# Optimization experiments

Measured on AMD Instinct MI355X. Metric: run time of the kernel, lower is better.

Reference implementation:

```python
import jax, jax.numpy as jnp
import numpy as np

N_NODES = 50000
N_EDGES = 600000
IN_C, HID, OUT_C, HEADS = 128, 64, 16, 4


def setup_inputs() -> dict:
    key = jax.random.key(0)
    ks = jax.random.split(key, 12)
    s = 1.0 / np.sqrt(HID)
    return {
        "x": jax.random.normal(ks[0], (N_NODES, IN_C), dtype=jnp.float32),
        "edge_index": jax.random.randint(ks[1], (2, N_EDGES), 0, N_NODES, dtype=jnp.int64),
        "W_lin": jax.random.normal(ks[2], (IN_C, HID), dtype=jnp.float32) / np.sqrt(IN_C),
        "b_lin": jnp.zeros((HID,), dtype=jnp.float32),
        "Wq": jax.random.normal(ks[3], (HID, HID), dtype=jnp.float32) * s,
        "bq": jnp.zeros((HID,), dtype=jnp.float32),
        "Wk": jax.random.normal(ks[4], (HID, HID), dtype=jnp.float32) * s,
        "bk": jnp.zeros((HID,), dtype=jnp.float32),
        "Wv": jax.random.normal(ks[5], (HID, HID), dtype=jnp.float32) * s,
        "bv": jnp.zeros((HID,), dtype=jnp.float32),
        "W_out": jax.random.normal(ks[6], (HID, OUT_C), dtype=jnp.float32) * s,
        "b_out": jnp.zeros((OUT_C,), dtype=jnp.float32),
    }


def _dna_conv(xs, src, dst, norm, Wq, bq, Wk, bk, Wv, bv):
    # xs: [N, L, C] stacked layer histories. Multi-head attention per edge:
    # query = target node's latest layer, keys/values = source node's full history.
    N, L, C = xs.shape
    d = C // HEADS
    q = (xs[:, -1] @ Wq + bq).reshape(N, HEADS, d)          # [N,H,d]
    k = (xs @ Wk + bk).reshape(N, L, HEADS, d)               # [N,L,H,d]
    v = (xs @ Wv + bv).reshape(N, L, HEADS, d)
    scores = jnp.einsum('ehd,elhd->ehl', q[dst], k[src]) / jnp.sqrt(jnp.float32(d))
    attn = jax.nn.softmax(scores, axis=-1)                   # softmax over layer history
    msg = jnp.einsum('ehl,elhd->ehd', attn, v[src]).reshape(-1, C)  # [E,C]
    msg = msg * norm[:, None]                                # GCN symmetric norm
    return jax.ops.segment_sum(msg, dst, num_segments=N)


def reference(x, edge_index, W_lin, b_lin, Wq, bq, Wk, bk, Wv, bv, W_out, b_out):
    N = x.shape[0]
    loop = jnp.arange(N, dtype=edge_index.dtype)
    src = jnp.concatenate([edge_index[0], loop])
    dst = jnp.concatenate([edge_index[1], loop])
    deg = jax.ops.segment_sum(jnp.ones_like(dst, dtype=x.dtype), dst, num_segments=N)
    dinv = jnp.where(deg > 0, jax.lax.rsqrt(jnp.maximum(deg, 1.0)), 0.0)
    norm = dinv[src] * dinv[dst]

    h = x @ W_lin + b_lin                                    # [N,HID]
    xs = h[:, None, :]
    for _ in range(3):
        out = _dna_conv(xs, src, dst, norm, Wq, bq, Wk, bk, Wv, bv)
        xs = jnp.concatenate([xs, out[:, None, :]], axis=1)
    return xs[:, -1] @ W_out + b_out                          # [N,OUT_C]
```

## Files before the change

### kernel.cpp

```cpp
#include <hip/hip_runtime.h>


__device__ inline unsigned short bf16_rne(float f) {
    unsigned int u = __float_as_uint(f);
    unsigned int r = u + 0x7FFFu + ((u >> 16) & 1u);
    return (unsigned short)(r >> 16);
}

__global__ __launch_bounds__(256) void hist_dst_k(const int* __restrict__ dst,
                                                  int* __restrict__ cnt, int E) {
    int e = blockIdx.x * 256 + threadIdx.x;
    if (e < E) atomicAdd(&cnt[dst[e]], 1);
}

__global__ __launch_bounds__(256) void scan1_k(const int* __restrict__ cnt,
                                               int* __restrict__ excl,
                                               int* __restrict__ aux,
                                               float* __restrict__ dinv, int N) {
    __shared__ int wtot[4];
    int b = blockIdx.x, t = threadIdx.x;
    int lane = t & 63, w = t >> 6;
    int base = b * 1024 + t * 4;
    int v0 = (base + 0 < N) ? cnt[base + 0] + 1 : 0;
    int v1 = (base + 1 < N) ? cnt[base + 1] + 1 : 0;
    int v2 = (base + 2 < N) ? cnt[base + 2] + 1 : 0;
    int v3 = (base + 3 < N) ? cnt[base + 3] + 1 : 0;
    if (base + 0 < N) dinv[base + 0] = rsqrtf((float)v0);
    if (base + 1 < N) dinv[base + 1] = rsqrtf((float)v1);
    if (base + 2 < N) dinv[base + 2] = rsqrtf((float)v2);
    if (base + 3 < N) dinv[base + 3] = rsqrtf((float)v3);
    int s = v0 + v1 + v2 + v3;
    int incl = s;
#pragma unroll
    for (int off = 1; off < 64; off <<= 1) {
        int u = __shfl_up(incl, off);
        if (lane >= off) incl += u;
    }
    if (lane == 63) wtot[w] = incl;
    __syncthreads();
    int wb = 0;
#pragma unroll
    for (int j = 0; j < 4; ++j) if (j < w) wb += wtot[j];
    int ex = wb + incl - s;
    if (base + 0 < N) excl[base + 0] = ex;
    if (base + 1 < N) excl[base + 1] = ex + v0;
    if (base + 2 < N) excl[base + 2] = ex + v0 + v1;
    if (base + 3 < N) excl[base + 3] = ex + v0 + v1 + v2;
    if (t == 0) aux[b] = wtot[0] + wtot[1] + wtot[2] + wtot[3];
}

__global__ __launch_bounds__(64) void scan_aux_k(int* __restrict__ aux, int nb,
                                                 int* __restrict__ total) {
    int lane = threadIdx.x;
    int v = (lane < nb) ? aux[lane] : 0;
    int incl = v;
#pragma unroll
    for (int off = 1; off < 64; off <<= 1) {
        int u = __shfl_up(incl, off);
        if (lane >= off) incl += u;
    }
    if (lane < nb) aux[lane] = incl - v;
    if (lane == 63) total[0] = incl;
}

__global__ __launch_bounds__(256) void scan_add_k(int* __restrict__ offs,
                                                  const int* __restrict__ aux,
                                                  int* __restrict__ cursor, int N) {
    int i = blockIdx.x * 256 + threadIdx.x;
    if (i < N) {
        int o = offs[i] + aux[i >> 10];
        offs[i] = o;
        cursor[i] = o;
    }
}

__global__ __launch_bounds__(256) void scatter_dst_k(const int* __restrict__ src,
                                                     const int* __restrict__ dst,
                                                     int* __restrict__ cursor,
                                                     int* __restrict__ src_sorted,
                                                     int E, int N) {
    int e = blockIdx.x * 256 + threadIdx.x;
    int M = E + N;
    if (e >= M) return;
    int s, d;
    if (e < E) { s = src[e]; d = dst[e]; }
    else       { s = d = e - E; }
    int pos = atomicAdd(&cursor[d], 1);
    src_sorted[pos] = s;
}

__global__ __launch_bounds__(256) void lin128_64_k(const float* __restrict__ x,
                                                   const float* __restrict__ W,
                                                   const float* __restrict__ b,
                                                   float* __restrict__ y, int N) {
    __shared__ float sW[128 * 64];
    __shared__ float sb[64];
    for (int i = threadIdx.x; i < 128 * 64; i += 256) sW[i] = W[i];
    if (threadIdx.x < 64) sb[threadIdx.x] = b[threadIdx.x];
    __syncthreads();
    int w = threadIdx.x >> 6, c = threadIdx.x & 63;
    int r0 = blockIdx.x * 16 + w * 4;
    if (r0 >= N) return;
    const float* xr[4];
#pragma unroll
    for (int j = 0; j < 4; ++j) {
        int r = r0 + j; if (r > N - 1) r = N - 1;
        xr[j] = x + (size_t)r * 128;
    }
    float acc[4];
#pragma unroll
    for (int j = 0; j < 4; ++j) acc[j] = sb[c];
    for (int k = 0; k < 128; ++k) {
        float wv = sW[k * 64 + c];
#pragma unroll
        for (int j = 0; j < 4; ++j) acc[j] = fmaf(xr[j][k], wv, acc[j]);
    }
#pragma unroll
    for (int j = 0; j < 4; ++j) {
        int r = r0 + j;
        if (r < N) y[(size_t)r * 64 + c] = acc[j];
    }
}

__global__ __launch_bounds__(1024) void qkv_pack0_k(const float* __restrict__ h,
                                                    const float* __restrict__ Wq, const float* __restrict__ bq,
                                                    const float* __restrict__ Wk, const float* __restrict__ bk,
                                                    const float* __restrict__ Wv, const float* __restrict__ bv,
                                                    const float* __restrict__ dinv,
                                                    float* __restrict__ q,
                                                    unsigned int* __restrict__ PL,
                                                    unsigned short* __restrict__ V0,
                                                    int N) {
    __shared__ float sW[3 * 64 * 64];
    __shared__ float rowS[16][64];
    int tid = threadIdx.x;
    for (int i = tid; i < 4096; i += 1024) {
        sW[i] = Wq[i]; sW[4096 + i] = Wk[i]; sW[8192 + i] = Wv[i];
    }
    __syncthreads();
    int w = tid >> 6, lane = tid & 63;
    int r = blockIdx.x * 16 + w;
    if (r >= N) return;
    rowS[w][lane] = h[(size_t)r * 64 + lane];
    float dr = dinv[r];
    float aq = bq[lane], ak = bk[lane], av = bv[lane];
#pragma unroll 8
    for (int k = 0; k < 64; ++k) {
        float xk = rowS[w][k];
        aq = fmaf(xk, sW[k * 64 + lane], aq);
        ak = fmaf(xk, sW[4096 + k * 64 + lane], ak);
        av = fmaf(xk, sW[8192 + k * 64 + lane], av);
    }
    q[(size_t)r * 64 + lane] = aq;
    unsigned short vb = bf16_rne(av * dr);
    PL[(size_t)r * 192 + lane] = (unsigned int)bf16_rne(ak) | ((unsigned int)vb << 16);
    V0[(size_t)r * 64 + lane] = vb;
}

template <int L, bool EMIT_OUT>
__global__ __launch_bounds__(1024) void attn_fused_k(const int* __restrict__ offs,
                                                     const int* __restrict__ src_sorted,
                                                     const float* __restrict__ dinv,
                                                     float* __restrict__ q,
                                                     unsigned int* __restrict__ PL,
                                                     const unsigned short* __restrict__ V0,
                                                     const float* __restrict__ WA, const float* __restrict__ bA,
                                                     const float* __restrict__ Wk, const float* __restrict__ bk,
                                                     const float* __restrict__ Wv, const float* __restrict__ bv,
                                                     float* __restrict__ out, int N) {
    constexpr int SWSZ = EMIT_OUT ? (64 * 16) : (3 * 64 * 64);
    __shared__ float sW[SWSZ];
    __shared__ float rowS[16][64];
    int tid = threadIdx.x;
    if (EMIT_OUT) {
        for (int i = tid; i < 64 * 16; i += 1024) sW[i] = WA[i];
    } else {
        for (int i = tid; i < 4096; i += 1024) {
            sW[i] = WA[i]; sW[4096 + i] = Wk[i]; sW[8192 + i] = Wv[i];
        }
    }
    __syncthreads();
    int w = tid >> 6, lane = tid & 63;
    int d = blockIdx.x * 16 + w;
    if (d >= N) return;

    int beg = offs[d], end = offs[d + 1];
    float qv = (L > 1) ? q[(size_t)d * 64 + lane] : 0.0f;
    float acc = 0.0f;

    for (int base = beg; base < end; base += 64) {
        int m = end - base;
        if (m > 64) m = 64;
        int sid = (base + lane < end) ? src_sorted[base + lane] : 0;
#pragma unroll 4
        for (int i = 0; i < m; ++i) {
            int s = __shfl(sid, i);
            if (L == 1) {
                acc += __uint_as_float((unsigned int)V0[(size_t)s * 64 + lane] << 16);
            } else if (L == 2) {
                const unsigned int* p = PL + (size_t)s * 192;
                unsigned int u0 = p[lane];
                unsigned int u1 = p[64 + lane];
                float k0 = __uint_as_float((u0 & 0xFFFFu) << 16);
                float v0 = __uint_as_float(u0 & 0xFFFF0000u);
                float k1 = __uint_as_float((u1 & 0xFFFFu) << 16);
                float v1 = __uint_as_float(u1 & 0xFFFF0000u);
                float p0 = qv * k0;
                float p1 = qv * k1;
#pragma unroll
                for (int mk = 8; mk >= 1; mk >>= 1) {
                    p0 += __shfl_xor(p0, mk);
                    p1 += __shfl_xor(p1, mk);
                }
                float e  = __expf((p1 - p0) * 0.25f);
                float w0 = __builtin_amdgcn_rcpf(1.0f + e);
                float w1 = 1.0f - w0;
                acc = fmaf(w0, v0, acc);
                acc = fmaf(w1, v1, acc);
            } else {
                const unsigned int* p = PL + (size_t)s * 192;
                unsigned int u0 = p[lane];
                unsigned int u1 = p[64 + lane];
                unsigned int u2 = p[128 + lane];
                float k0 = __uint_as_float((u0 & 0xFFFFu) << 16);
                float v0 = __uint_as_float(u0 & 0xFFFF0000u);
                float k1 = __uint_as_float((u1 & 0xFFFFu) << 16);
                float v1 = __uint_as_float(u1 & 0xFFFF0000u);
                float k2 = __uint_as_float((u2 & 0xFFFFu) << 16);
                float v2 = __uint_as_float(u2 & 0xFFFF0000u);
                float p0 = qv * k0;
                float p1 = qv * k1;
                float p2 = qv * k2;
#pragma unroll
                for (int mk = 8; mk >= 1; mk >>= 1) {
                    p0 += __shfl_xor(p0, mk);
                    p1 += __shfl_xor(p1, mk);
                    p2 += __shfl_xor(p2, mk);
                }
                float s0 = p0 * 0.25f, s1 = p1 * 0.25f, s2 = p2 * 0.25f;
                float mx = fmaxf(fmaxf(s0, s1), s2);
                float w0 = __expf(s0 - mx);
                float w1 = __expf(s1 - mx);
                float w2 = __expf(s2 - mx);
                float inv = __builtin_amdgcn_rcpf(w0 + w1 + w2);
                float msg = w0 * v0;
                msg = fmaf(w1, v1, msg);
                msg = fmaf(w2, v2, msg);
                acc = fmaf(msg, inv, acc);
            }
        }
    }

    float dr = dinv[d];
    float rv = acc * dr;
    rowS[w][lane] = rv;

    if (EMIT_OUT) {
        int co = lane & 15;
        float ao = bA[co];
#pragma unroll 8
        for (int k = 0; k < 64; ++k) ao = fmaf(rowS[w][k], sW[k * 16 + co], ao);
        if (lane < 16) out[(size_t)d * 16 + co] = ao;
    } else {
        float aq = bA[lane], ak = bk[lane], av = bv[lane];
#pragma unroll 8
        for (int k = 0; k < 64; ++k) {
            float xk = rowS[w][k];
            aq = fmaf(xk, sW[k * 64 + lane], aq);
            ak = fmaf(xk, sW[4096 + k * 64 + lane], ak);
            av = fmaf(xk, sW[8192 + k * 64 + lane], av);
        }
        q[(size_t)d * 64 + lane] = aq;
        PL[(size_t)d * 192 + L * 64 + lane] =
            (unsigned int)bf16_rne(ak) | ((unsigned int)bf16_rne(av * dr) << 16);
    }
}

extern "C" void kernel_launch(void* const* d_in, const int* in_sizes, int n_in,
                              void* d_out, int out_size, void* d_ws, size_t ws_size,
                              hipStream_t stream) {
    const float* x     = (const float*)d_in[0];
    const int*   ei    = (const int*)d_in[1];
    const float* W_lin = (const float*)d_in[2];
    const float* b_lin = (const float*)d_in[3];
    const float* Wq    = (const float*)d_in[4];
    const float* bq    = (const float*)d_in[5];
    const float* Wk    = (const float*)d_in[6];
    const float* bk    = (const float*)d_in[7];
    const float* Wv    = (const float*)d_in[8];
    const float* bv    = (const float*)d_in[9];
    const float* W_out = (const float*)d_in[10];
    const float* b_out = (const float*)d_in[11];
    float* out = (float*)d_out;

    const int N = in_sizes[0] / 128;
    const int E = in_sizes[1] / 2;
    const int M = E + N;
    const int* srcp = ei;
    const int* dstp = ei + E;

    char* wsb = (char*)d_ws;
    float*          dinv       = (float*)wsb;           wsb += (size_t)N * sizeof(float);
    int*            cnt        = (int*)wsb;             wsb += (size_t)N * sizeof(int);
    int*            offs       = (int*)wsb;             wsb += (size_t)(N + 1) * sizeof(int);
    int*            cursor     = (int*)wsb;             wsb += (size_t)N * sizeof(int);
    int*            aux        = (int*)wsb;             wsb += 64 * sizeof(int);
    int*            src_sorted = (int*)wsb;             wsb += (size_t)M * sizeof(int);
    float*          qb         = (float*)wsb;           wsb += (size_t)N * 64 * sizeof(float);
    unsigned int*   PL         = (unsigned int*)wsb;    wsb += (size_t)N * 192 * sizeof(unsigned int);
    unsigned short* V0p        = (unsigned short*)wsb;  wsb += (size_t)N * 64 * sizeof(unsigned short);
    float*          hA         = (float*)wsb;

    const int gN   = (N + 255) / 256;
    const int gE   = (E + 255) / 256;
    const int gM   = (M + 255) / 256;
    const int g16  = (N + 15) / 16;
    const int nb   = (N + 1023) / 1024;

    hipMemsetAsync(cnt, 0, (size_t)N * sizeof(int), stream);
    hist_dst_k<<<gE, 256, 0, stream>>>(dstp, cnt, E);
    scan1_k<<<nb, 256, 0, stream>>>(cnt, offs, aux, dinv, N);
    scan_aux_k<<<1, 64, 0, stream>>>(aux, nb, offs + N);
    scan_add_k<<<gN, 256, 0, stream>>>(offs, aux, cursor, N);
    scatter_dst_k<<<gM, 256, 0, stream>>>(srcp, dstp, cursor, src_sorted, E, N);

    lin128_64_k<<<g16, 256, 0, stream>>>(x, W_lin, b_lin, hA, N);
    qkv_pack0_k<<<g16, 1024, 0, stream>>>(hA, Wq, bq, Wk, bk, Wv, bv, dinv,
                                          qb, PL, V0p, N);

    attn_fused_k<1, false><<<g16, 1024, 0, stream>>>(offs, src_sorted, dinv, qb, PL, V0p,
                                                     Wq, bq, Wk, bk, Wv, bv, out, N);
    attn_fused_k<2, false><<<g16, 1024, 0, stream>>>(offs, src_sorted, dinv, qb, PL, V0p,
                                                     Wq, bq, Wk, bk, Wv, bv, out, N);
    attn_fused_k<3, true><<<g16, 1024, 0, stream>>>(offs, src_sorted, dinv, qb, PL, V0p,
                                                    W_out, b_out, Wk, bk, Wv, bv, out, N);
}
```

Before: 510.0 us.

## Switch to edge-parallel strip attention with atomics and separate projection kernels

Replaces the per-destination-wavefront fused attention+projection kernels with an edge-strip kernel. Each 16-lane group processes 8 consecutive sorted edges using vectorized uint4 loads and 4-lane head reductions, flushing partial sums with float atomics when the destination changes. The QKV projections move to a separate register-resident-weight kernel using readlane broadcasts, with the query scale folded into q. The output projection also becomes its own kernel. The aim is to balance load across skewed degrees and widen memory accesses. The cost is extra kernels, memsets, a dst_sorted array and atomic traffic.

Measured after the change: 691.7 us. 1.36x slower.

```diff
diff --git a/kernel.cpp b/kernel.cpp
--- a/kernel.cpp
+++ b/kernel.cpp
@@ -1,11 +1,15 @@
 #include <hip/hip_runtime.h>
 
+
+#define SEDGE 8
 
 __device__ inline unsigned short bf16_rne(float f) {
     unsigned int u = __float_as_uint(f);
     unsigned int r = u + 0x7FFFu + ((u >> 16) & 1u);
     return (unsigned short)(r >> 16);
 }
+__device__ inline float kf(unsigned int u) { return __uint_as_float(u << 16); }
+__device__ inline float vf(unsigned int u) { return __uint_as_float(u & 0xFFFF0000u); }
 
 __global__ __launch_bounds__(256) void hist_dst_k(const int* __restrict__ dst,
                                                   int* __restrict__ cnt, int E) {
@@ -78,6 +82,7 @@
                                                      const int* __restrict__ dst,
                                                      int* __restrict__ cursor,
                                                      int* __restrict__ src_sorted,
+                                                     int* __restrict__ dst_sorted,
                                                      int E, int N) {
     int e = blockIdx.x * 256 + threadIdx.x;
     int M = E + N;
@@ -87,6 +92,7 @@
     else       { s = d = e - E; }
     int pos = atomicAdd(&cursor[d], 1);
     src_sorted[pos] = s;
+    dst_sorted[pos] = d;
 }
 
 __global__ __launch_bounds__(256) void lin128_64_k(const float* __restrict__ x,
@@ -122,158 +128,167 @@
     }
 }
 
-__global__ __launch_bounds__(1024) void qkv_pack0_k(const float* __restrict__ h,
-                                                    const float* __restrict__ Wq, const float* __restrict__ bq,
-                                                    const float* __restrict__ Wk, const float* __restrict__ bk,
-                                                    const float* __restrict__ Wv, const float* __restrict__ bv,
+template <bool WRITE_V0>
+__global__ __launch_bounds__(192) void proj_qkv_k(const float* __restrict__ X,
+                                                  const float* __restrict__ Wq, const float* __restrict__ bq,
+                                                  const float* __restrict__ Wk, const float* __restrict__ bk,
+                                                  const float* __restrict__ Wv, const float* __restrict__ bv,
+                                                  const float* __restrict__ dinv,
+                                                  float* __restrict__ q,
+                                                  unsigned int* __restrict__ PL,
+                                                  unsigned short* __restrict__ V0,
+                                                  int N, int l, int RPB) {
+    int w = threadIdx.x >> 6;
+    int c = threadIdx.x & 63;
+    const float* W = (w == 0) ? Wq : (w == 1) ? Wk : Wv;
+    const float* B = (w == 0) ? bq : (w == 1) ? bk : bv;
+    float wr[64];
+#pragma unroll
+    for (int k = 0; k < 64; ++k) wr[k] = W[k * 64 + c];
+    float bias = B[c];
+    int r0 = blockIdx.x * RPB;
+    int r1 = r0 + RPB; if (r1 > N) r1 = N;
+    unsigned short* PLh = (unsigned short*)PL;
+    for (int r = r0; r < r1; ++r) {
+        float xv = X[(size_t)r * 64 + c];
+        float a = bias;
+#pragma unroll
+        for (int k = 0; k < 64; ++k) {
+            float xk = __int_as_float(__builtin_amdgcn_readlane(__float_as_int(xv), k));
+            a = fmaf(xk, wr[k], a);
+        }
+        if (w == 0) {
+            q[(size_t)r * 64 + c] = a * 0.25f;
+        } else if (w == 1) {
+            PLh[((size_t)r * 192 + l * 64 + c) * 2] = bf16_rne(a);
+        } else {
+            unsigned short vb = bf16_rne(a * dinv[r]);
+            PLh[((size_t)r * 192 + l * 64 + c) * 2 + 1] = vb;
+            if (WRITE_V0) V0[(size_t)r * 64 + c] = vb;
+        }
+    }
+}
+
+template <int L>
+__global__ __launch_bounds__(256) void attn_strip_k(const int* __restrict__ src_sorted,
+                                                    const int* __restrict__ dst_sorted,
                                                     const float* __restrict__ dinv,
-                                                    float* __restrict__ q,
-                                                    unsigned int* __restrict__ PL,
-                                                    unsigned short* __restrict__ V0,
-                                                    int N) {
-    __shared__ float sW[3 * 64 * 64];
-    __shared__ float rowS[16][64];
-    int tid = threadIdx.x;
-    for (int i = tid; i < 4096; i += 1024) {
-        sW[i] = Wq[i]; sW[4096 + i] = Wk[i]; sW[8192 + i] = Wv[i];
-    }
-    __syncthreads();
-    int w = tid >> 6, lane = tid & 63;
-    int r = blockIdx.x * 16 + w;
-    if (r >= N) return;
-    rowS[w][lane] = h[(size_t)r * 64 + lane];
-    float dr = dinv[r];
-    float aq = bq[lane], ak = bk[lane], av = bv[lane];
-#pragma unroll 8
-    for (int k = 0; k < 64; ++k) {
-        float xk = rowS[w][k];
-        aq = fmaf(xk, sW[k * 64 + lane], aq);
-        ak = fmaf(xk, sW[4096 + k * 64 + lane], ak);
-        av = fmaf(xk, sW[8192 + k * 64 + lane], av);
-    }
-    q[(size_t)r * 64 + lane] = aq;
-    unsigned short vb = bf16_rne(av * dr);
-    PL[(size_t)r * 192 + lane] = (unsigned int)bf16_rne(ak) | ((unsigned int)vb << 16);
-    V0[(size_t)r * 64 + lane] = vb;
-}
-
-template <int L, bool EMIT_OUT>
-__global__ __launch_bounds__(1024) void attn_fused_k(const int* __restrict__ offs,
-                                                     const int* __restrict__ src_sorted,
-                                                     const float* __restrict__ dinv,
-                                                     float* __restrict__ q,
-                                                     unsigned int* __restrict__ PL,
-                                                     const unsigned short* __restrict__ V0,
-                                                     const float* __restrict__ WA, const float* __restrict__ bA,
-                                                     const float* __restrict__ Wk, const float* __restrict__ bk,
-                                                     const float* __restrict__ Wv, const float* __restrict__ bv,
-                                                     float* __restrict__ out, int N) {
-    constexpr int SWSZ = EMIT_OUT ? (64 * 16) : (3 * 64 * 64);
-    __shared__ float sW[SWSZ];
-    __shared__ float rowS[16][64];
-    int tid = threadIdx.x;
-    if (EMIT_OUT) {
-        for (int i = tid; i < 64 * 16; i += 1024) sW[i] = WA[i];
-    } else {
-        for (int i = tid; i < 4096; i += 1024) {
-            sW[i] = WA[i]; sW[4096 + i] = Wk[i]; sW[8192 + i] = Wv[i];
+                                                    const float* __restrict__ q,
+                                                    const uint4* __restrict__ PL4,
+                                                    const unsigned short* __restrict__ V0,
+                                                    float* __restrict__ out, int M) {
+    int g  = (blockIdx.x * 256 + threadIdx.x) >> 4;
+    int gl = threadIdx.x & 15;
+    long base = (long)g * SEDGE;
+    if (base >= M) return;
+
+    int   cur_d = -1;
+    float dv = 0.f;
+    float4 qv = make_float4(0.f, 0.f, 0.f, 0.f);
+    float a0 = 0.f, a1 = 0.f, a2 = 0.f, a3 = 0.f;
+
+    for (int i = 0; i < SEDGE; ++i) {
+        long pos = base + i;
+        if (pos >= M) break;
+        int s = src_sorted[pos];
+        int d = dst_sorted[pos];
+        if (d != cur_d) {
+            if (cur_d >= 0) {
+                float* op = out + (size_t)cur_d * 64 + gl * 4;
+                atomicAdd(op + 0, a0 * dv);
+                atomicAdd(op + 1, a1 * dv);
+                atomicAdd(op + 2, a2 * dv);
+                atomicAdd(op + 3, a3 * dv);
+                a0 = a1 = a2 = a3 = 0.f;
+            }
+            cur_d = d;
+            dv = dinv[d];
+            if (L > 1) qv = *(const float4*)(q + (size_t)d * 64 + gl * 4);
         }
-    }
-    __syncthreads();
-    int w = tid >> 6, lane = tid & 63;
-    int d = blockIdx.x * 16 + w;
-    if (d >= N) return;
-
-    int beg = offs[d], end = offs[d + 1];
-    float qv = (L > 1) ? q[(size_t)d * 64 + lane] : 0.0f;
-    float acc = 0.0f;
-
-    for (int base = beg; base < end; base += 64) {
-        int m = end - base;
-        if (m > 64) m = 64;
-        int sid = (base + lane < end) ? src_sorted[base + lane] : 0;
-#pragma unroll 4
-        for (int i = 0; i < m; ++i) {
-            int s = __shfl(sid, i);
-            if (L == 1) {
-                acc += __uint_as_float((unsigned int)V0[(size_t)s * 64 + lane] << 16);
-            } else if (L == 2) {
-                const unsigned int* p = PL + (size_t)s * 192;
-                unsigned int u0 = p[lane];
-                unsigned int u1 = p[64 + lane];
-                float k0 = __uint_as_float((u0 & 0xFFFFu) << 16);
-                float v0 = __uint_as_float(u0 & 0xFFFF0000u);
-                float k1 = __uint_as_float((u1 & 0xFFFFu) << 16);
-                float v1 = __uint_as_float(u1 & 0xFFFF0000u);
-                float p0 = qv * k0;
-                float p1 = qv * k1;
-#pragma unroll
-                for (int mk = 8; mk >= 1; mk >>= 1) {
-                    p0 += __shfl_xor(p0, mk);
-                    p1 += __shfl_xor(p1, mk);
-                }
-                float e  = __expf((p1 - p0) * 0.25f);
-                float w0 = __builtin_amdgcn_rcpf(1.0f + e);
-                float w1 = 1.0f - w0;
-                acc = fmaf(w0, v0, acc);
-                acc = fmaf(w1, v1, acc);
+        if (L == 1) {
+            uint2 raw = *(const uint2*)(V0 + (size_t)s * 64 + gl * 4);
+            a0 += kf(raw.x);  a1 += vf(raw.x) ;
+            a2 += kf(raw.y);  a3 += vf(raw.y);
+        } else {
+            const uint4* p = PL4 + (size_t)s * 48 + gl;
+            uint4 u0 = p[0];
+            uint4 u1 = p[16];
+            uint4 u2 = u0;
+            if (L > 2) u2 = p[32];
+            float p0 = qv.x * kf(u0.x);
+            p0 = fmaf(qv.y, kf(u0.y), p0);
+            p0 = fmaf(qv.z, kf(u0.z), p0);
+            p0 = fmaf(qv.w, kf(u0.w), p0);
+            float p1 = qv.x * kf(u1.x);
+            p1 = fmaf(qv.y, kf(u1.y), p1);
+            p1 = fmaf(qv.z, kf(u1.z), p1);
+            p1 = fmaf(qv.w, kf(u1.w), p1);
+            float p2 = 0.f;
+            if (L > 2) {
+                p2 = qv.x * kf(u2.x);
+                p2 = fmaf(qv.y, kf(u2.y), p2);
+                p2 = fmaf(qv.z, kf(u2.z), p2);
+                p2 = fmaf(qv.w, kf(u2.w), p2);
+            }
+            p0 += __shfl_xor(p0, 1); p0 += __shfl_xor(p0, 2);
+            p1 += __shfl_xor(p1, 1); p1 += __shfl_xor(p1, 2);
+            if (L > 2) { p2 += __shfl_xor(p2, 1); p2 += __shfl_xor(p2, 2); }
+            float w0, w1, w2;
+            if (L == 2) {
+                float e = __expf(p1 - p0);
+                w0 = __builtin_amdgcn_rcpf(1.0f + e);
+                w1 = 1.0f - w0;
+                w2 = 0.f;
             } else {
-                const unsigned int* p = PL + (size_t)s * 192;
-                unsigned int u0 = p[lane];
-                unsigned int u1 = p[64 + lane];
-                unsigned int u2 = p[128 + lane];
-                float k0 = __uint_as_float((u0 & 0xFFFFu) << 16);
-                float v0 = __uint_as_float(u0 & 0xFFFF0000u);
-                float k1 = __uint_as_float((u1 & 0xFFFFu) << 16);
-                float v1 = __uint_as_float(u1 & 0xFFFF0000u);
-                float k2 = __uint_as_float((u2 & 0xFFFFu) << 16);
-                float v2 = __uint_as_float(u2 & 0xFFFF0000u);
-                float p0 = qv * k0;
-                float p1 = qv * k1;
-                float p2 = qv * k2;
-#pragma unroll
-                for (int mk = 8; mk >= 1; mk >>= 1) {
-                    p0 += __shfl_xor(p0, mk);
-                    p1 += __shfl_xor(p1, mk);
-                    p2 += __shfl_xor(p2, mk);
-                }
-                float s0 = p0 * 0.25f, s1 = p1 * 0.25f, s2 = p2 * 0.25f;
-                float mx = fmaxf(fmaxf(s0, s1), s2);
-                float w0 = __expf(s0 - mx);
-                float w1 = __expf(s1 - mx);
-                float w2 = __expf(s2 - mx);
-                float inv = __builtin_amdgcn_rcpf(w0 + w1 + w2);
-                float msg = w0 * v0;
-                msg = fmaf(w1, v1, msg);
-                msg = fmaf(w2, v2, msg);
-                acc = fmaf(msg, inv, acc);
+                float mx = fmaxf(fmaxf(p0, p1), p2);
+                float e0 = __expf(p0 - mx);
+                float e1 = __expf(p1 - mx);
+                float e2 = __expf(p2 - mx);
+                float inv = __builtin_amdgcn_rcpf(e0 + e1 + e2);
+                w0 = e0 * inv; w1 = e1 * inv; w2 = e2 * inv;
+            }
+            a0 = fmaf(w0, vf(u0.x), a0);
+            a1 = fmaf(w0, vf(u0.y), a1);
+            a2 = fmaf(w0, vf(u0.z), a2);
+            a3 = fmaf(w0, vf(u0.w), a3);
+            a0 = fmaf(w1, vf(u1.x), a0);
+            a1 = fmaf(w1, vf(u1.y), a1);
+            a2 = fmaf(w1, vf(u1.z), a2);
+            a3 = fmaf(w1, vf(u1.w), a3);
+            if (L > 2) {
+                a0 = fmaf(w2, vf(u2.x), a0);
+                a1 = fmaf(w2, vf(u2.y), a1);
+                a2 = fmaf(w2, vf(u2.z), a2);
+                a3 = fmaf(w2, vf(u2.w), a3);
             }
         }
     }
-
-    float dr = dinv[d];
-    float rv = acc * dr;
-    rowS[w][lane] = rv;
-
-    if (EMIT_OUT) {
-        int co = lane & 15;
-        float ao = bA[co];
-#pragma unroll 8
-        for (int k = 0; k < 64; ++k) ao = fmaf(rowS[w][k], sW[k * 16 + co], ao);
-        if (lane < 16) out[(size_t)d * 16 + co] = ao;
-    } else {
-        float aq = bA[lane], ak = bk[lane], av = bv[lane];
-#pragma unroll 8
-        for (int k = 0; k < 64; ++k) {
-            float xk = rowS[w][k];
-            aq = fmaf(xk, sW[k * 64 + lane], aq);
-            ak = fmaf(xk, sW[4096 + k * 64 + lane], ak);
-            av = fmaf(xk, sW[8192 + k * 64 + lane], av);
-        }
-        q[(size_t)d * 64 + lane] = aq;
-        PL[(size_t)d * 192 + L * 64 + lane] =
-            (unsigned int)bf16_rne(ak) | ((unsigned int)bf16_rne(av * dr) << 16);
-    }
+    if (cur_d >= 0) {
+        float* op = out + (size_t)cur_d * 64 + gl * 4;
+        atomicAdd(op + 0, a0 * dv);
+        atomicAdd(op + 1, a1 * dv);
+        atomicAdd(op + 2, a2 * dv);
+        atomicAdd(op + 3, a3 * dv);
+    }
+}
+
+__global__ __launch_bounds__(256) void out_proj_k(const float* __restrict__ xs,
+                                                  const float* __restrict__ W,
+                                                  const float* __restrict__ b,
+                                                  float* __restrict__ y, int N) {
+    __shared__ float sW[64 * 16];
+    __shared__ float sb[16];
+    for (int i = threadIdx.x; i < 64 * 16; i += 256) sW[i] = W[i];
+    if (threadIdx.x < 16) sb[threadIdx.x] = b[threadIdx.x];
+    __syncthreads();
+    int row = blockIdx.x * 16 + (threadIdx.x >> 4);
+    int c   = threadIdx.x & 15;
+    if (row >= N) return;
+    const float* xr = xs + (size_t)row * 64;
+    float acc = sb[c];
+#pragma unroll 16
+    for (int k = 0; k < 64; ++k) acc = fmaf(xr[k], sW[k * 16 + c], acc);
+    y[(size_t)row * 16 + c] = acc;
 }
 
 extern "C" void kernel_launch(void* const* d_in, const int* in_sizes, int n_in,
@@ -306,32 +321,47 @@
     int*            cursor     = (int*)wsb;             wsb += (size_t)N * sizeof(int);
     int*            aux        = (int*)wsb;             wsb += 64 * sizeof(int);
     int*            src_sorted = (int*)wsb;             wsb += (size_t)M * sizeof(int);
+    int*            dst_sorted = (int*)wsb;             wsb += (size_t)M * sizeof(int);
     float*          qb         = (float*)wsb;           wsb += (size_t)N * 64 * sizeof(float);
     unsigned int*   PL         = (unsigned int*)wsb;    wsb += (size_t)N * 192 * sizeof(unsigned int);
     unsigned short* V0p        = (unsigned short*)wsb;  wsb += (size_t)N * 64 * sizeof(unsigned short);
-    float*          hA         = (float*)wsb;
+    float*          hA         = (float*)wsb;           wsb += (size_t)N * 64 * sizeof(float);
+    float*          outb       = (float*)wsb;
 
     const int gN   = (N + 255) / 256;
     const int gE   = (E + 255) / 256;
     const int gM   = (M + 255) / 256;
     const int g16  = (N + 15) / 16;
     const int nb   = (N + 1023) / 1024;
+    const int RPB  = 16;
+    const int gP   = (N + RPB - 1) / RPB;
+    const int ngrp = (M + SEDGE - 1) / SEDGE;
+    const int gA   = (ngrp + 15) / 16;
 
     hipMemsetAsync(cnt, 0, (size_t)N * sizeof(int), stream);
     hist_dst_k<<<gE, 256, 0, stream>>>(dstp, cnt, E);
     scan1_k<<<nb, 256, 0, stream>>>(cnt, offs, aux, dinv, N);
     scan_aux_k<<<1, 64, 0, stream>>>(aux, nb, offs + N);
     scan_add_k<<<gN, 256, 0, stream>>>(offs, aux, cursor, N);
-    scatter_dst_k<<<gM, 256, 0, stream>>>(srcp, dstp, cursor, src_sorted, E, N);
+    scatter_dst_k<<<gM, 256, 0, stream>>>(srcp, dstp, cursor, src_sorted, dst_sorted, E, N);
 
     lin128_64_k<<<g16, 256, 0, stream>>>(x, W_lin, b_lin, hA, N);
-    qkv_pack0_k<<<g16, 1024, 0, stream>>>(hA, Wq, bq, Wk, bk, Wv, bv, dinv,
-                                          qb, PL, V0p, N);
-
-    attn_fused_k<1, false><<<g16, 1024, 0, stream>>>(offs, src_sorted, dinv, qb, PL, V0p,
-                                                     Wq, bq, Wk, bk, Wv, bv, out, N);
-    attn_fused_k<2, false><<<g16, 1024, 0, stream>>>(offs, src_sorted, dinv, qb, PL, V0p,
-                                                     Wq, bq, Wk, bk, Wv, bv, out, N);
-    attn_fused_k<3, true><<<g16, 1024, 0, stream>>>(offs, src_sorted, dinv, qb, PL, V0p,
-                                                    W_out, b_out, Wk, bk, Wv, bv, out, N);
-}
+    proj_qkv_k<true><<<gP, 192, 0, stream>>>(hA, Wq, bq, Wk, bk, Wv, bv, dinv,
+                                             qb, PL, V0p, N, 0, RPB);
+
+    const uint4* PL4 = (const uint4*)PL;
+    const size_t outBytes = (size_t)N * 64 * sizeof(float);
+
+    hipMemsetAsync(outb, 0, outBytes, stream);
+    attn_strip_k<1><<<gA, 256, 0, stream>>>(src_sorted, dst_sorted, dinv, qb, PL4, V0p, outb, M);
+    proj_qkv_k<false><<<gP, 192, 0, stream>>>(outb, Wq, bq, Wk, bk, Wv, bv, dinv,
+                                              qb, PL, V0p, N, 1, RPB);
+    hipMemsetAsync(outb, 0, outBytes, stream);
+    attn_strip_k<2><<<gA, 256, 0, stream>>>(src_sorted, dst_sorted, dinv, qb, PL4, V0p, outb, M);
+    proj_qkv_k<false><<<gP, 192, 0, stream>>>(outb, Wq, bq, Wk, bk, Wv, bv, dinv,
+                                              qb, PL, V0p, N, 2, RPB);
+    hipMemsetAsync(outb, 0, outBytes, stream);
+    attn_strip_k<3><<<gA, 256, 0, stream>>>(src_sorted, dst_sorted, dinv, qb, PL4, V0p, outb, M);
+
+    out_proj_k<<<g16, 256, 0, stream>>>(outb, W_out, b_out, out, N);
+}
```

## Split fused attention+projection into small-block attention and register-weight projection kernels

Applied to the files above, without the earlier changes.

Replaces the 1024-thread fused attention kernels, which each held a 48KB LDS weight tile, with a 256-thread gather/attention kernel plus a separate 192-thread projection kernel. The projection kernel keeps one weight column per thread in registers and broadcasts row elements with readlane. The 1/sqrt(d) scale is folded into q at projection time, and the output projection becomes its own kernel. The aim is higher occupancy for the latency-bound edge gather. The cost is extra launches and an intermediate buffer that goes through global memory between stages.

Result: faster. 495.2 us (-2.9%).

```diff
diff --git a/kernel.cpp b/kernel.cpp
--- a/kernel.cpp
+++ b/kernel.cpp
@@ -122,70 +122,61 @@
     }
 }
 
-__global__ __launch_bounds__(1024) void qkv_pack0_k(const float* __restrict__ h,
-                                                    const float* __restrict__ Wq, const float* __restrict__ bq,
-                                                    const float* __restrict__ Wk, const float* __restrict__ bk,
-                                                    const float* __restrict__ Wv, const float* __restrict__ bv,
-                                                    const float* __restrict__ dinv,
-                                                    float* __restrict__ q,
-                                                    unsigned int* __restrict__ PL,
-                                                    unsigned short* __restrict__ V0,
-                                                    int N) {
-    __shared__ float sW[3 * 64 * 64];
-    __shared__ float rowS[16][64];
-    int tid = threadIdx.x;
-    for (int i = tid; i < 4096; i += 1024) {
-        sW[i] = Wq[i]; sW[4096 + i] = Wk[i]; sW[8192 + i] = Wv[i];
-    }
-    __syncthreads();
-    int w = tid >> 6, lane = tid & 63;
-    int r = blockIdx.x * 16 + w;
-    if (r >= N) return;
-    rowS[w][lane] = h[(size_t)r * 64 + lane];
-    float dr = dinv[r];
-    float aq = bq[lane], ak = bk[lane], av = bv[lane];
-#pragma unroll 8
-    for (int k = 0; k < 64; ++k) {
-        float xk = rowS[w][k];
-        aq = fmaf(xk, sW[k * 64 + lane], aq);
-        ak = fmaf(xk, sW[4096 + k * 64 + lane], ak);
-        av = fmaf(xk, sW[8192 + k * 64 + lane], av);
-    }
-    q[(size_t)r * 64 + lane] = aq;
-    unsigned short vb = bf16_rne(av * dr);
-    PL[(size_t)r * 192 + lane] = (unsigned int)bf16_rne(ak) | ((unsigned int)vb << 16);
-    V0[(size_t)r * 64 + lane] = vb;
-}
-
-template <int L, bool EMIT_OUT>
-__global__ __launch_bounds__(1024) void attn_fused_k(const int* __restrict__ offs,
-                                                     const int* __restrict__ src_sorted,
-                                                     const float* __restrict__ dinv,
-                                                     float* __restrict__ q,
-                                                     unsigned int* __restrict__ PL,
-                                                     const unsigned short* __restrict__ V0,
-                                                     const float* __restrict__ WA, const float* __restrict__ bA,
-                                                     const float* __restrict__ Wk, const float* __restrict__ bk,
-                                                     const float* __restrict__ Wv, const float* __restrict__ bv,
-                                                     float* __restrict__ out, int N) {
-    constexpr int SWSZ = EMIT_OUT ? (64 * 16) : (3 * 64 * 64);
-    __shared__ float sW[SWSZ];
-    __shared__ float rowS[16][64];
-    int tid = threadIdx.x;
-    if (EMIT_OUT) {
-        for (int i = tid; i < 64 * 16; i += 1024) sW[i] = WA[i];
-    } else {
-        for (int i = tid; i < 4096; i += 1024) {
-            sW[i] = WA[i]; sW[4096 + i] = Wk[i]; sW[8192 + i] = Wv[i];
+template <bool WRITE_V0>
+__global__ __launch_bounds__(192) void proj_qkv_k(const float* __restrict__ X,
+                                                  const float* __restrict__ Wq, const float* __restrict__ bq,
+                                                  const float* __restrict__ Wk, const float* __restrict__ bk,
+                                                  const float* __restrict__ Wv, const float* __restrict__ bv,
+                                                  const float* __restrict__ dinv,
+                                                  float* __restrict__ q,
+                                                  unsigned int* __restrict__ PL,
+                                                  unsigned short* __restrict__ V0,
+                                                  int N, int l, int RPB) {
+    int w = threadIdx.x >> 6;
+    int c = threadIdx.x & 63;
+    const float* W = (w == 0) ? Wq : (w == 1) ? Wk : Wv;
+    const float* B = (w == 0) ? bq : (w == 1) ? bk : bv;
+    float wr[64];
+#pragma unroll
+    for (int k = 0; k < 64; ++k) wr[k] = W[k * 64 + c];
+    float bias = B[c];
+    int r0 = blockIdx.x * RPB;
+    int r1 = r0 + RPB; if (r1 > N) r1 = N;
+    unsigned short* PLh = (unsigned short*)PL;
+    for (int r = r0; r < r1; ++r) {
+        float xv = X[(size_t)r * 64 + c];
+        float a = bias;
+#pragma unroll
+        for (int k = 0; k < 64; ++k) {
+            float xk = __int_as_float(__builtin_amdgcn_readlane(__float_as_int(xv), k));
+            a = fmaf(xk, wr[k], a);
         }
-    }
-    __syncthreads();
-    int w = tid >> 6, lane = tid & 63;
-    int d = blockIdx.x * 16 + w;
+        if (w == 0) {
+            q[(size_t)r * 64 + c] = a * 0.25f;
+        } else if (w == 1) {
+            PLh[((size_t)r * 192 + l * 64 + c) * 2] = bf16_rne(a);
+        } else {
+            unsigned short vb = bf16_rne(a * dinv[r]);
+            PLh[((size_t)r * 192 + l * 64 + c) * 2 + 1] = vb;
+            if (WRITE_V0) V0[(size_t)r * 64 + c] = vb;
+        }
+    }
+}
+
+template <int L>
+__global__ __launch_bounds__(256) void attn_dst_k(const int* __restrict__ offs,
+                                                  const int* __restrict__ src_sorted,
+                                                  const float* __restrict__ dinv,
+                                                  const float* __restrict__ q,
+                                                  const unsigned int* __restrict__ PL,
+                                                  const unsigned short* __restrict__ V0,
+                                                  float* __restrict__ out,
+                                                  int N) {
+    int d    = (blockIdx.x * 256 + threadIdx.x) >> 6;
+    int lane = threadIdx.x & 63;
     if (d >= N) return;
-
     int beg = offs[d], end = offs[d + 1];
-    float qv = (L > 1) ? q[(size_t)d * 64 + lane] : 0.0f;
+    float qv  = (L > 1) ? q[(size_t)d * 64 + lane] : 0.0f;
     float acc = 0.0f;
 
     for (int base = beg; base < end; base += 64) {
@@ -212,7 +203,7 @@
                     p0 += __shfl_xor(p0, mk);
                     p1 += __shfl_xor(p1, mk);
                 }
-                float e  = __expf((p1 - p0) * 0.25f);
+                float e  = __expf(p1 - p0);
                 float w0 = __builtin_amdgcn_rcpf(1.0f + e);
                 float w1 = 1.0f - w0;
                 acc = fmaf(w0, v0, acc);
@@ -237,11 +228,10 @@
                     p1 += __shfl_xor(p1, mk);
                     p2 += __shfl_xor(p2, mk);
                 }
-                float s0 = p0 * 0.25f, s1 = p1 * 0.25f, s2 = p2 * 0.25f;
-                float mx = fmaxf(fmaxf(s0, s1), s2);
-                float w0 = __expf(s0 - mx);
-                float w1 = __expf(s1 - mx);
-                float w2 = __expf(s2 - mx);
+                float mx = fmaxf(fmaxf(p0, p1), p2);
+                float w0 = __expf(p0 - mx);
+                float w1 = __expf(p1 - mx);
+                float w2 = __expf(p2 - mx);
                 float inv = __builtin_amdgcn_rcpf(w0 + w1 + w2);
                 float msg = w0 * v0;
                 msg = fmaf(w1, v1, msg);
@@ -250,30 +240,26 @@
             }
         }
     }
-
-    float dr = dinv[d];
-    float rv = acc * dr;
-    rowS[w][lane] = rv;
-
-    if (EMIT_OUT) {
-        int co = lane & 15;
-        float ao = bA[co];
-#pragma unroll 8
-        for (int k = 0; k < 64; ++k) ao = fmaf(rowS[w][k], sW[k * 16 + co], ao);
-        if (lane < 16) out[(size_t)d * 16 + co] = ao;
-    } else {
-        float aq = bA[lane], ak = bk[lane], av = bv[lane];
-#pragma unroll 8
-        for (int k = 0; k < 64; ++k) {
-            float xk = rowS[w][k];
-            aq = fmaf(xk, sW[k * 64 + lane], aq);
-            ak = fmaf(xk, sW[4096 + k * 64 + lane], ak);
-            av = fmaf(xk, sW[8192 + k * 64 + lane], av);
-        }
-        q[(size_t)d * 64 + lane] = aq;
-        PL[(size_t)d * 192 + L * 64 + lane] =
-            (unsigned int)bf16_rne(ak) | ((unsigned int)bf16_rne(av * dr) << 16);
-    }
+    out[(size_t)d * 64 + lane] = acc * dinv[d];
+}
+
+__global__ __launch_bounds__(256) void out_proj_k(const float* __restrict__ xs,
+                                                  const float* __restrict__ W,
+                                                  const float* __restrict__ b,
+                                                  float* __restrict__ y, int N) {
+    __shared__ float sW[64 * 16];
+    __shared__ float sb[16];
+    for (int i = threadIdx.x; i < 64 * 16; i += 256) sW[i] = W[i];
+    if (threadIdx.x < 16) sb[threadIdx.x] = b[threadIdx.x];
+    __syncthreads();
+    int row = blockIdx.x * 16 + (threadIdx.x >> 4);
+    int c   = threadIdx.x & 15;
+    if (row >= N) return;
+    const float* xr = xs + (size_t)row * 64;
+    float acc = sb[c];
+#pragma unroll 16
+    for (int k = 0; k < 64; ++k) acc = fmaf(xr[k], sW[k * 16 + c], acc);
+    y[(size_t)row * 16 + c] = acc;
 }
 
 extern "C" void kernel_launch(void* const* d_in, const int* in_sizes, int n_in,
@@ -309,13 +295,17 @@
     float*          qb         = (float*)wsb;           wsb += (size_t)N * 64 * sizeof(float);
     unsigned int*   PL         = (unsigned int*)wsb;    wsb += (size_t)N * 192 * sizeof(unsigned int);
     unsigned short* V0p        = (unsigned short*)wsb;  wsb += (size_t)N * 64 * sizeof(unsigned short);
-    float*          hA         = (float*)wsb;
+    float*          hA         = (float*)wsb;           wsb += (size_t)N * 64 * sizeof(float);
+    float*          outb       = (float*)wsb;
 
     const int gN   = (N + 255) / 256;
     const int gE   = (E + 255) / 256;
     const int gM   = (M + 255) / 256;
+    const int gRow = (N + 3) / 4;
     const int g16  = (N + 15) / 16;
     const int nb   = (N + 1023) / 1024;
+    const int RPB  = 16;
+    const int gP   = (N + RPB - 1) / RPB;
 
     hipMemsetAsync(cnt, 0, (size_t)N * sizeof(int), stream);
     hist_dst_k<<<gE, 256, 0, stream>>>(dstp, cnt, E);
@@ -325,13 +315,16 @@
     scatter_dst_k<<<gM, 256, 0, stream>>>(srcp, dstp, cursor, src_sorted, E, N);
 
     lin128_64_k<<<g16, 256, 0, stream>>>(x, W_lin, b_lin, hA, N);
-    qkv_pack0_k<<<g16, 1024, 0, stream>>>(hA, Wq, bq, Wk, bk, Wv, bv, dinv,
-                                          qb, PL, V0p, N);
-
-    attn_fused_k<1, false><<<g16, 1024, 0, stream>>>(offs, src_sorted, dinv, qb, PL, V0p,
-                                                     Wq, bq, Wk, bk, Wv, bv, out, N);
-    attn_fused_k<2, false><<<g16, 1024, 0, stream>>>(offs, src_sorted, dinv, qb, PL, V0p,
-                                                     Wq, bq, Wk, bk, Wv, bv, out, N);
-    attn_fused_k<3, true><<<g16, 1024, 0, stream>>>(offs, src_sorted, dinv, qb, PL, V0p,
-                                                    W_out, b_out, Wk, bk, Wv, bv, out, N);
-}
+    proj_qkv_k<true><<<gP, 192, 0, stream>>>(hA, Wq, bq, Wk, bk, Wv, bv, dinv,
+                                             qb, PL, V0p, N, 0, RPB);
+
+    attn_dst_k<1><<<gRow, 256, 0, stream>>>(offs, src_sorted, dinv, qb, PL, V0p, outb, N);
+    proj_qkv_k<false><<<gP, 192, 0, stream>>>(outb, Wq, bq, Wk, bk, Wv, bv, dinv,
+                                              qb, PL, V0p, N, 1, RPB);
+    attn_dst_k<2><<<gRow, 256, 0, stream>>>(offs, src_sorted, dinv, qb, PL, V0p, outb, N);
+    proj_qkv_k<false><<<gP, 192, 0, stream>>>(outb, Wq, bq, Wk, bk, Wv, bv, dinv,
+                                              qb, PL, V0p, N, 2, RPB);
+    attn_dst_k<3><<<gRow, 256, 0, stream>>>(offs, src_sorted, dinv, qb, PL, V0p, outb, N);
+
+    out_proj_k<<<g16, 256, 0, stream>>>(outb, W_out, b_out, out, N);
+}
```
